# Performance work log

Hardware: AMD Instinct MI355X
Metric: run time of the kernel (lower is better)

## Reference

```python
import jax, jax.numpy as jnp
import numpy as np

N_NODES = 100_000
N_EDGES = 1_600_000
F_DIM = 32


def setup_inputs() -> dict:
    key = jax.random.key(0)
    k1, k2, k3 = jax.random.split(key, 3)
    x = jax.random.normal(k1, (N_NODES, F_DIM), dtype=jnp.float32)
    edge_index = jax.random.randint(k2, (2, N_EDGES), 0, N_NODES, dtype=jnp.int64)
    edge_weight = jax.random.uniform(k3, (N_EDGES,), dtype=jnp.float32)
    w_mp = jnp.array([0.5], dtype=jnp.float32)  # learned scalar parameter
    return {"x": x, "edge_index": edge_index, "edge_weight": edge_weight, "w_mp": w_mp}


def reference(x, edge_index, edge_weight, w_mp):
    # message: ea = w_mp * x[src] * edge_weight  (shape [E, F])
    # aggregate: sum messages into target nodes (aggr='add', source_to_target)
    src = edge_index[0]
    dst = edge_index[1]
    ea = (w_mp * x[src]) * edge_weight[:, None]          # [E, F]
    out = jax.ops.segment_sum(ea, dst, num_segments=x.shape[0])  # [N, F]
    return out
```

## Files before the change

### kernel.cpp

```cpp
#include <hip/hip_runtime.h>


constexpr int N_NODES = 100000;
constexpr int N_EDGES = 1600000;
constexpr int F_DIM   = 32;

constexpr int NPB_C = 256;
constexpr int NB_C  = (N_NODES + NPB_C - 1) / NPB_C;
constexpr int CAP_C = 4608;

constexpr int BIN_THREADS = 512;
constexpr int BIN_BLOCKS  = 256;
constexpr int BIN_CHUNK   = N_EDGES / BIN_BLOCKS;
constexpr int BIN_EPT     = (BIN_CHUNK + BIN_THREADS - 1) / BIN_THREADS;

constexpr int AGG_THREADS = 1024;
constexpr int GRPT = (CAP_C + AGG_THREADS - 1) / AGG_THREADS;

constexpr size_t WS_CURSOR  = 0;
constexpr size_t WS_RECORDS = 4096;
constexpr size_t WS_NEEDED  = WS_RECORDS + (size_t)NB_C * CAP_C * 8;

__global__ __launch_bounds__(BIN_THREADS) void bin_edges(
    const int* __restrict__ src, const int* __restrict__ dst,
    const float* __restrict__ ew, const float* __restrict__ w_mp,
    int* __restrict__ gcursor, uint2* __restrict__ records)
{
    __shared__ int lhist[NB_C];
    __shared__ int lbase[NB_C];
    if (threadIdx.x < NB_C) lhist[threadIdx.x] = 0;
    __syncthreads();

    const float w = w_mp[0];
    const int base_e = blockIdx.x * BIN_CHUNK;
    const int e_end  = min(base_e + BIN_CHUNK, N_EDGES);
    int   bkt[BIN_EPT];
    uint2 rec[BIN_EPT];

    #pragma unroll
    for (int i = 0; i < BIN_EPT; ++i) {
        int e = base_e + threadIdx.x + i * BIN_THREADS;
        bkt[i] = -1;
        if (e < e_end) {
            int d = dst[e];
            int b = d >> 8;
            bkt[i] = b;
            rec[i].x = __float_as_uint(w * ew[e]);
            rec[i].y = (unsigned)src[e] | ((unsigned)(d & 255) << 24);
            atomicAdd(&lhist[b], 1);
        }
    }
    __syncthreads();

    if (threadIdx.x < NB_C) {
        int c = lhist[threadIdx.x];
        int base = c ? atomicAdd(&gcursor[threadIdx.x], c) : 0;
        lbase[threadIdx.x] = threadIdx.x * CAP_C + base;
        lhist[threadIdx.x] = 0;
    }
    __syncthreads();

    #pragma unroll
    for (int i = 0; i < BIN_EPT; ++i) {
        int b = bkt[i];
        if (b >= 0) {
            int pos = lbase[b] + atomicAdd(&lhist[b], 1);
            if (pos < (b + 1) * CAP_C)
                records[pos] = rec[i];
        }
    }
}

__global__ __launch_bounds__(AGG_THREADS) void sort_gather(
    const int*   __restrict__ gcursor,
    const uint2* __restrict__ records,
    const float* __restrict__ x,
    float*       __restrict__ out)
{
    __shared__ uint2 sorted[CAP_C];
    __shared__ int   hist[NPB_C];
    __shared__ int   offs[NPB_C + 1];
    __shared__ int   cursor[NPB_C];

    const int coarse = blockIdx.x;
    const int t      = threadIdx.x;

    if (t < NPB_C) hist[t] = 0;
    __syncthreads();

    const int rbase = coarse * CAP_C;
    const int cnt   = min(gcursor[coarse], CAP_C);

    uint2 rec[GRPT];
    #pragma unroll
    for (int i = 0; i < GRPT; ++i) {
        int j = t + i * AGG_THREADS;
        rec[i].y = 0xFFFFFFFFu;
        if (j < cnt) {
            rec[i] = records[rbase + j];
            atomicAdd(&hist[rec[i].y >> 24], 1);
        }
    }
    __syncthreads();

    if (t < 64) {
        const int b4 = t * 4;
        int h0 = hist[b4], h1 = hist[b4 + 1], h2 = hist[b4 + 2], h3 = hist[b4 + 3];
        int s   = h0 + h1 + h2 + h3;
        int inc = s;
        #pragma unroll
        for (int d = 1; d < 64; d <<= 1) {
            int o = __shfl_up(inc, d, 64);
            if (t >= d) inc += o;
        }
        int base = inc - s;
        offs[b4]     = base;
        offs[b4 + 1] = base + h0;
        offs[b4 + 2] = base + h0 + h1;
        offs[b4 + 3] = base + h0 + h1 + h2;
        cursor[b4]     = base;
        cursor[b4 + 1] = base + h0;
        cursor[b4 + 2] = base + h0 + h1;
        cursor[b4 + 3] = base + h0 + h1 + h2;
        if (t == 63) offs[NPB_C] = inc;
    }
    __syncthreads();

    #pragma unroll
    for (int i = 0; i < GRPT; ++i) {
        if (rec[i].y != 0xFFFFFFFFu) {
            int slot = atomicAdd(&cursor[rec[i].y >> 24], 1);
            sorted[slot] = rec[i];
        }
    }
    __syncthreads();

    const int qq = (t & 7) * 4;
    #pragma unroll
    for (int p = 0; p < 2; ++p) {
        const int node  = p * (AGG_THREADS / 8) + (t >> 3);
        const int gnode = coarse * NPB_C + node;
        if (gnode >= N_NODES) continue;

        int j  = offs[node];
        int je = offs[node + 1];
        float4 acc = make_float4(0.f, 0.f, 0.f, 0.f);

        for (; j + 4 <= je; j += 4) {
            uint2 r0 = sorted[j + 0];
            uint2 r1 = sorted[j + 1];
            uint2 r2 = sorted[j + 2];
            uint2 r3 = sorted[j + 3];
            const float4 v0 = *reinterpret_cast<const float4*>(
                x + (size_t)(r0.y & 0xFFFFFFu) * F_DIM + qq);
            const float4 v1 = *reinterpret_cast<const float4*>(
                x + (size_t)(r1.y & 0xFFFFFFu) * F_DIM + qq);
            const float4 v2 = *reinterpret_cast<const float4*>(
                x + (size_t)(r2.y & 0xFFFFFFu) * F_DIM + qq);
            const float4 v3 = *reinterpret_cast<const float4*>(
                x + (size_t)(r3.y & 0xFFFFFFu) * F_DIM + qq);
            float c0 = __uint_as_float(r0.x), c1 = __uint_as_float(r1.x);
            float c2 = __uint_as_float(r2.x), c3 = __uint_as_float(r3.x);
            acc.x += c0 * v0.x + c1 * v1.x + c2 * v2.x + c3 * v3.x;
            acc.y += c0 * v0.y + c1 * v1.y + c2 * v2.y + c3 * v3.y;
            acc.z += c0 * v0.z + c1 * v1.z + c2 * v2.z + c3 * v3.z;
            acc.w += c0 * v0.w + c1 * v1.w + c2 * v2.w + c3 * v3.w;
        }
        for (; j < je; ++j) {
            uint2 r = sorted[j];
            float c = __uint_as_float(r.x);
            const float4 v = *reinterpret_cast<const float4*>(
                x + (size_t)(r.y & 0xFFFFFFu) * F_DIM + qq);
            acc.x += c * v.x;
            acc.y += c * v.y;
            acc.z += c * v.z;
            acc.w += c * v.w;
        }
        *reinterpret_cast<float4*>(out + (size_t)gnode * F_DIM + qq) = acc;
    }
}

__global__ __launch_bounds__(256) void gnn_scatter_atomic(
    const float* __restrict__ x, const int* __restrict__ src,
    const int* __restrict__ dst, const float* __restrict__ ew,
    const float* __restrict__ w_mp, float* __restrict__ out)
{
    const float w = w_mp[0];
    int gid = blockIdx.x * blockDim.x + threadIdx.x;
    int e = gid >> 3;
    int qq = (gid & 7) * 4;
    if (e >= N_EDGES) return;
    int s = src[e];
    int d = dst[e];
    float c = w * ew[e];
    const float4 xv = *reinterpret_cast<const float4*>(x + (size_t)s * F_DIM + qq);
    float* op = out + (size_t)d * F_DIM + qq;
    atomicAdd(op + 0, c * xv.x);
    atomicAdd(op + 1, c * xv.y);
    atomicAdd(op + 2, c * xv.z);
    atomicAdd(op + 3, c * xv.w);
}

extern "C" void kernel_launch(void* const* d_in, const int* in_sizes, int n_in,
                              void* d_out, int out_size, void* d_ws, size_t ws_size,
                              hipStream_t stream) {
    const float* x    = (const float*)d_in[0];
    const int*   ei   = (const int*)d_in[1];
    const float* ew   = (const float*)d_in[2];
    const float* w_mp = (const float*)d_in[3];
    float* out = (float*)d_out;

    const int* src = ei;
    const int* dst = ei + N_EDGES;

    if (ws_size < WS_NEEDED) {
        hipMemsetAsync(d_out, 0, (size_t)out_size * sizeof(float), stream);
        int total = N_EDGES * 8;
        gnn_scatter_atomic<<<(total + 255) / 256, 256, 0, stream>>>(
            x, src, dst, ew, w_mp, out);
        return;
    }

    char* ws = (char*)d_ws;
    int*   gcursor = (int*)(ws + WS_CURSOR);
    uint2* records = (uint2*)(ws + WS_RECORDS);

    hipMemsetAsync(gcursor, 0, NB_C * sizeof(int), stream);
    bin_edges<<<BIN_BLOCKS, BIN_THREADS, 0, stream>>>(src, dst, ew, w_mp,
                                                      gcursor, records);
    sort_gather<<<NB_C, AGG_THREADS, 0, stream>>>(gcursor, records, x, out);
}
```

Before: 125.6 us.

## Fuse binning and gather into one cooperative kernel with per-block bucket runs

Merges the edge-binning and sort/gather passes into a single cooperative kernel separated by a grid-wide sync, with a two-kernel fallback if the cooperative launch fails. Binning no longer uses global atomics or a memset: each binning block writes into its own fixed-capacity run (48 slots) per coarse bucket and records a count, and the gather block reads the 256 runs for its bucket. This removes the global cursor atomics, the memset and one launch, but the cooperative launch needs all 391 blocks of 1024 threads resident at once. The per-run capacity of 48 can silently drop edges if a run overflows.

```diff
diff --git a/kernel.cpp b/kernel.cpp
--- a/kernel.cpp
+++ b/kernel.cpp
@@ -1,156 +1,129 @@
 #include <hip/hip_runtime.h>
+#include <hip/hip_cooperative_groups.h>
+
+namespace cg = cooperative_groups;
 
 
 constexpr int N_NODES = 100000;
 constexpr int N_EDGES = 1600000;
 constexpr int F_DIM   = 32;
 
-constexpr int NPB_C = 256;
-constexpr int NB_C  = (N_NODES + NPB_C - 1) / NPB_C;
-constexpr int CAP_C = 4608;
-
-constexpr int BIN_THREADS = 512;
-constexpr int BIN_BLOCKS  = 256;
-constexpr int BIN_CHUNK   = N_EDGES / BIN_BLOCKS;
-constexpr int BIN_EPT     = (BIN_CHUNK + BIN_THREADS - 1) / BIN_THREADS;
-
-constexpr int AGG_THREADS = 1024;
-constexpr int GRPT = (CAP_C + AGG_THREADS - 1) / AGG_THREADS;
-
-constexpr size_t WS_CURSOR  = 0;
-constexpr size_t WS_RECORDS = 4096;
-constexpr size_t WS_NEEDED  = WS_RECORDS + (size_t)NB_C * CAP_C * 8;
-
-__global__ __launch_bounds__(BIN_THREADS) void bin_edges(
+constexpr int NPB   = 256;
+constexpr int NB    = (N_NODES + NPB - 1) / NPB;
+constexpr int BINB  = 256;
+constexpr int CHUNK = N_EDGES / BINB;
+constexpr int BCAP  = 48;
+constexpr int SCAP  = 4608;
+constexpr int THREADS = 1024;
+
+constexpr size_t WS_COUNTS  = 0;
+constexpr size_t WS_RECORDS = 512 * 1024;
+constexpr size_t WS_NEEDED  = WS_RECORDS + (size_t)NB * BINB * BCAP * 8;
+
+struct P2 {
+    uint2 sorted[SCAP];
+    int   hist[NPB];
+    int   offs[NPB + 1];
+    int   cursor[NPB];
+    int   cnts[BINB];
+};
+union Smem {
+    int lcur[NB];
+    P2  p2;
+};
+
+__device__ __forceinline__ void phase1_bin(
+    Smem& s, int b, int t,
     const int* __restrict__ src, const int* __restrict__ dst,
-    const float* __restrict__ ew, const float* __restrict__ w_mp,
-    int* __restrict__ gcursor, uint2* __restrict__ records)
-{
-    __shared__ int lhist[NB_C];
-    __shared__ int lbase[NB_C];
-    if (threadIdx.x < NB_C) lhist[threadIdx.x] = 0;
-    __syncthreads();
-
-    const float w = w_mp[0];
-    const int base_e = blockIdx.x * BIN_CHUNK;
-    const int e_end  = min(base_e + BIN_CHUNK, N_EDGES);
-    int   bkt[BIN_EPT];
-    uint2 rec[BIN_EPT];
-
-    #pragma unroll
-    for (int i = 0; i < BIN_EPT; ++i) {
-        int e = base_e + threadIdx.x + i * BIN_THREADS;
-        bkt[i] = -1;
-        if (e < e_end) {
-            int d = dst[e];
-            int b = d >> 8;
-            bkt[i] = b;
-            rec[i].x = __float_as_uint(w * ew[e]);
-            rec[i].y = (unsigned)src[e] | ((unsigned)(d & 255) << 24);
-            atomicAdd(&lhist[b], 1);
-        }
-    }
-    __syncthreads();
-
-    if (threadIdx.x < NB_C) {
-        int c = lhist[threadIdx.x];
-        int base = c ? atomicAdd(&gcursor[threadIdx.x], c) : 0;
-        lbase[threadIdx.x] = threadIdx.x * CAP_C + base;
-        lhist[threadIdx.x] = 0;
-    }
-    __syncthreads();
-
-    #pragma unroll
-    for (int i = 0; i < BIN_EPT; ++i) {
-        int b = bkt[i];
-        if (b >= 0) {
-            int pos = lbase[b] + atomicAdd(&lhist[b], 1);
-            if (pos < (b + 1) * CAP_C)
-                records[pos] = rec[i];
-        }
-    }
-}
-
-__global__ __launch_bounds__(AGG_THREADS) void sort_gather(
-    const int*   __restrict__ gcursor,
-    const uint2* __restrict__ records,
-    const float* __restrict__ x,
-    float*       __restrict__ out)
-{
-    __shared__ uint2 sorted[CAP_C];
-    __shared__ int   hist[NPB_C];
-    __shared__ int   offs[NPB_C + 1];
-    __shared__ int   cursor[NPB_C];
-
-    const int coarse = blockIdx.x;
-    const int t      = threadIdx.x;
-
-    if (t < NPB_C) hist[t] = 0;
-    __syncthreads();
-
-    const int rbase = coarse * CAP_C;
-    const int cnt   = min(gcursor[coarse], CAP_C);
-
-    uint2 rec[GRPT];
-    #pragma unroll
-    for (int i = 0; i < GRPT; ++i) {
-        int j = t + i * AGG_THREADS;
-        rec[i].y = 0xFFFFFFFFu;
-        if (j < cnt) {
-            rec[i] = records[rbase + j];
-            atomicAdd(&hist[rec[i].y >> 24], 1);
-        }
-    }
+    const float* __restrict__ ew, float w,
+    int* __restrict__ counts, uint2* __restrict__ recs)
+{
+    for (int i = t; i < NB; i += THREADS) s.lcur[i] = 0;
+    __syncthreads();
+
+    const int e0 = b * CHUNK;
+    for (int i = t; i < CHUNK; i += THREADS) {
+        int e = e0 + i;
+        int d = dst[e];
+        int k = d >> 8;
+        uint2 r;
+        r.x = __float_as_uint(w * ew[e]);
+        r.y = (unsigned)src[e] | ((unsigned)(d & 255) << 24);
+        int pos = atomicAdd(&s.lcur[k], 1);
+        if (pos < BCAP)
+            recs[((size_t)k * BINB + b) * BCAP + pos] = r;
+    }
+    __syncthreads();
+
+    for (int k = t; k < NB; k += THREADS)
+        counts[b * NB + k] = min(s.lcur[k], BCAP);
+}
+
+__device__ __forceinline__ void phase2_gather(
+    Smem& s, int k, int t,
+    const int* __restrict__ counts, const uint2* __restrict__ recs,
+    const float* __restrict__ x, float* __restrict__ out)
+{
+    P2& p = s.p2;
+    if (t < BINB) p.cnts[t] = counts[t * NB + k];
+    if (t < NPB)  p.hist[t] = 0;
+    __syncthreads();
+
+    const int run = t >> 2;
+    const int sub = t & 3;
+    const uint2* rb = recs + ((size_t)k * BINB + run) * BCAP;
+    const int rc = p.cnts[run];
+    for (int i = sub; i < rc; i += 4)
+        atomicAdd(&p.hist[rb[i].y >> 24], 1);
     __syncthreads();
 
     if (t < 64) {
         const int b4 = t * 4;
-        int h0 = hist[b4], h1 = hist[b4 + 1], h2 = hist[b4 + 2], h3 = hist[b4 + 3];
-        int s   = h0 + h1 + h2 + h3;
-        int inc = s;
+        int h0 = p.hist[b4], h1 = p.hist[b4 + 1];
+        int h2 = p.hist[b4 + 2], h3 = p.hist[b4 + 3];
+        int ssum = h0 + h1 + h2 + h3;
+        int inc = ssum;
         #pragma unroll
         for (int d = 1; d < 64; d <<= 1) {
             int o = __shfl_up(inc, d, 64);
             if (t >= d) inc += o;
         }
-        int base = inc - s;
-        offs[b4]     = base;
-        offs[b4 + 1] = base + h0;
-        offs[b4 + 2] = base + h0 + h1;
-        offs[b4 + 3] = base + h0 + h1 + h2;
-        cursor[b4]     = base;
-        cursor[b4 + 1] = base + h0;
-        cursor[b4 + 2] = base + h0 + h1;
-        cursor[b4 + 3] = base + h0 + h1 + h2;
-        if (t == 63) offs[NPB_C] = inc;
-    }
-    __syncthreads();
-
-    #pragma unroll
-    for (int i = 0; i < GRPT; ++i) {
-        if (rec[i].y != 0xFFFFFFFFu) {
-            int slot = atomicAdd(&cursor[rec[i].y >> 24], 1);
-            sorted[slot] = rec[i];
-        }
+        int base = inc - ssum;
+        p.offs[b4]     = base;
+        p.offs[b4 + 1] = base + h0;
+        p.offs[b4 + 2] = base + h0 + h1;
+        p.offs[b4 + 3] = base + h0 + h1 + h2;
+        p.cursor[b4]     = base;
+        p.cursor[b4 + 1] = base + h0;
+        p.cursor[b4 + 2] = base + h0 + h1;
+        p.cursor[b4 + 3] = base + h0 + h1 + h2;
+        if (t == 63) p.offs[NPB] = inc;
+    }
+    __syncthreads();
+
+    for (int i = sub; i < rc; i += 4) {
+        uint2 r = rb[i];
+        int slot = atomicAdd(&p.cursor[r.y >> 24], 1);
+        if (slot < SCAP) p.sorted[slot] = r;
     }
     __syncthreads();
 
     const int qq = (t & 7) * 4;
     #pragma unroll
-    for (int p = 0; p < 2; ++p) {
-        const int node  = p * (AGG_THREADS / 8) + (t >> 3);
-        const int gnode = coarse * NPB_C + node;
+    for (int ph = 0; ph < 2; ++ph) {
+        const int node  = ph * (THREADS / 8) + (t >> 3);
+        const int gnode = k * NPB + node;
         if (gnode >= N_NODES) continue;
 
-        int j  = offs[node];
-        int je = offs[node + 1];
+        int j  = min(p.offs[node], SCAP);
+        int je = min(p.offs[node + 1], SCAP);
         float4 acc = make_float4(0.f, 0.f, 0.f, 0.f);
 
         for (; j + 4 <= je; j += 4) {
-            uint2 r0 = sorted[j + 0];
-            uint2 r1 = sorted[j + 1];
-            uint2 r2 = sorted[j + 2];
-            uint2 r3 = sorted[j + 3];
+            uint2 r0 = p.sorted[j + 0];
+            uint2 r1 = p.sorted[j + 1];
+            uint2 r2 = p.sorted[j + 2];
+            uint2 r3 = p.sorted[j + 3];
             const float4 v0 = *reinterpret_cast<const float4*>(
                 x + (size_t)(r0.y & 0xFFFFFFu) * F_DIM + qq);
             const float4 v1 = *reinterpret_cast<const float4*>(
@@ -167,7 +140,7 @@
             acc.w += c0 * v0.w + c1 * v1.w + c2 * v2.w + c3 * v3.w;
         }
         for (; j < je; ++j) {
-            uint2 r = sorted[j];
+            uint2 r = p.sorted[j];
             float c = __uint_as_float(r.x);
             const float4 v = *reinterpret_cast<const float4*>(
                 x + (size_t)(r.y & 0xFFFFFFu) * F_DIM + qq);
@@ -178,6 +151,38 @@
         }
         *reinterpret_cast<float4*>(out + (size_t)gnode * F_DIM + qq) = acc;
     }
+}
+
+__global__ __launch_bounds__(THREADS, 8) void fused_coop(
+    const int* __restrict__ src, const int* __restrict__ dst,
+    const float* __restrict__ ew, const float* __restrict__ w_mp,
+    int* __restrict__ counts, uint2* __restrict__ recs,
+    const float* __restrict__ x, float* __restrict__ out)
+{
+    __shared__ Smem s;
+    const int b = blockIdx.x;
+    const int t = threadIdx.x;
+    if (b < BINB)
+        phase1_bin(s, b, t, src, dst, ew, w_mp[0], counts, recs);
+    cg::this_grid().sync();
+    phase2_gather(s, b, t, counts, recs, x, out);
+}
+
+__global__ __launch_bounds__(THREADS, 8) void bin_part(
+    const int* __restrict__ src, const int* __restrict__ dst,
+    const float* __restrict__ ew, const float* __restrict__ w_mp,
+    int* __restrict__ counts, uint2* __restrict__ recs)
+{
+    __shared__ Smem s;
+    phase1_bin(s, blockIdx.x, threadIdx.x, src, dst, ew, w_mp[0], counts, recs);
+}
+
+__global__ __launch_bounds__(THREADS, 8) void gather_part(
+    const int* __restrict__ counts, const uint2* __restrict__ recs,
+    const float* __restrict__ x, float* __restrict__ out)
+{
+    __shared__ Smem s;
+    phase2_gather(s, blockIdx.x, threadIdx.x, counts, recs, x, out);
 }
 
 __global__ __launch_bounds__(256) void gnn_scatter_atomic(
@@ -222,11 +227,15 @@
     }
 
     char* ws = (char*)d_ws;
-    int*   gcursor = (int*)(ws + WS_CURSOR);
-    uint2* records = (uint2*)(ws + WS_RECORDS);
-
-    hipMemsetAsync(gcursor, 0, NB_C * sizeof(int), stream);
-    bin_edges<<<BIN_BLOCKS, BIN_THREADS, 0, stream>>>(src, dst, ew, w_mp,
-                                                      gcursor, records);
-    sort_gather<<<NB_C, AGG_THREADS, 0, stream>>>(gcursor, records, x, out);
-}
+    int*   counts = (int*)(ws + WS_COUNTS);
+    uint2* recs   = (uint2*)(ws + WS_RECORDS);
+
+    void* args[] = {(void*)&src, (void*)&dst, (void*)&ew, (void*)&w_mp,
+                    (void*)&counts, (void*)&recs, (void*)&x, (void*)&out};
+    hipError_t st = hipLaunchCooperativeKernel(
+        (const void*)fused_coop, dim3(NB), dim3(THREADS), args, 0, stream);
+    if (st != hipSuccess) {
+        bin_part<<<BINB, THREADS, 0, stream>>>(src, dst, ew, w_mp, counts, recs);
+        gather_part<<<NB, THREADS, 0, stream>>>(counts, recs, x, out);
+    }
+}
```

Result: slower. 188.2 us (+49.8%).
